# Kernel optimization log

Measured on AMD Instinct MI355X. Metric: run time of the kernel, lower is better.

The kernel has to match this reference:

```python
import jax, jax.numpy as jnp
import numpy as np

N_NODES = 100000
N_EDGES = 1600000
N_GRAPHS = 64
IN_CH = 4
HID = 64
EPS = 1e-5


def setup_inputs() -> dict:
    key = jax.random.key(0)
    ks = jax.random.split(key, 12)
    x = jax.random.normal(ks[0], (N_NODES, IN_CH), dtype=jnp.float32)
    edge_index = jax.random.randint(ks[1], (2, N_EDGES), 0, N_NODES, dtype=jnp.int32)
    batch = jnp.sort(jax.random.randint(ks[2], (N_NODES,), 0, N_GRAPHS, dtype=jnp.int32))
    s = 1.0 / np.sqrt(IN_CH)
    W_l = jax.random.uniform(ks[3], (IN_CH, HID), jnp.float32, -s, s)
    b_l = jnp.zeros((HID,), jnp.float32)
    W_r = jax.random.uniform(ks[4], (IN_CH, HID), jnp.float32, -s, s)
    b_r = jnp.zeros((HID,), jnp.float32)
    att = jax.random.normal(ks[5], (HID,), jnp.float32) / np.sqrt(HID)
    conv_bias = jnp.zeros((HID,), jnp.float32)
    ln_w = jnp.ones((HID,), jnp.float32)
    ln_b = jnp.zeros((HID,), jnp.float32)
    s2 = 1.0 / np.sqrt(HID)
    lin_w = jax.random.uniform(ks[6], (HID, 1), jnp.float32, -s2, s2)
    lin_b = jnp.zeros((1,), jnp.float32)
    return dict(x=x, edge_index=edge_index, batch=batch, W_l=W_l, b_l=b_l,
                W_r=W_r, b_r=b_r, att=att, conv_bias=conv_bias,
                ln_w=ln_w, ln_b=ln_b, lin_w=lin_w, lin_b=lin_b)


def reference(x, edge_index, batch, W_l, b_l, W_r, b_r, att, conv_bias, ln_w, ln_b, lin_w, lin_b):
    src, dst = edge_index[0], edge_index[1]  # messages flow src -> dst
    # GATv2Conv (heads=1, no self loops)
    xl = x @ W_l + b_l  # source-side transform [N, HID]
    xr = x @ W_r + b_r  # target-side transform [N, HID]
    h = xl[src] + xr[dst]                                    # [E, HID]
    e = jnp.sum(jax.nn.leaky_relu(h, 0.2) * att, axis=-1)    # [E]
    # segment softmax over incoming edges of each target node
    m = jax.ops.segment_max(e, dst, num_segments=N_NODES)
    ex = jnp.exp(e - m[dst])
    denom = jax.ops.segment_sum(ex, dst, num_segments=N_NODES)
    alpha = ex / denom[dst]                                  # [E]
    out = jax.ops.segment_sum(alpha[:, None] * xl[src], dst, num_segments=N_NODES)
    out = out + conv_bias
    out = jax.nn.relu(out)
    # PyG LayerNorm, graph mode, batch=None -> normalize over all nodes & channels
    mu = jnp.mean(out)
    var = jnp.var(out)
    out = (out - mu) / jnp.sqrt(var + EPS) * ln_w + ln_b
    # (dropout omitted: deterministic reference / eval mode)
    # global mean pool over graphs
    cnt = jax.ops.segment_sum(jnp.ones((N_NODES,), out.dtype), batch, num_segments=N_GRAPHS)
    pooled = jax.ops.segment_sum(out, batch, num_segments=N_GRAPHS) / jnp.maximum(cnt, 1.0)[:, None]
    y = pooled @ lin_w + lin_b
    return jax.nn.sigmoid(y)  # [N_GRAPHS, 1]
```

## Files before the change

### kernel.cpp

```cpp
#include <hip/hip_runtime.h>
#include <math.h>

#define N_NODES 100000
#define N_EDGES 1600000
#define N_GRAPHS 64
#define HID 64
#define LN_EPS 1e-5f
#define NB_SCAN ((N_NODES + 255) / 256)
#define KD_BLOCKS 2048
#define KD_WAVES (KD_BLOCKS * 4)
#define KD_CHUNK ((N_NODES + KD_WAVES - 1) / KD_WAVES)

__device__ __forceinline__ float waveReduceSum(float v) {
#pragma unroll
    for (int off = 32; off > 0; off >>= 1)
        v += __shfl_xor(v, off, 64);
    return v;
}

__device__ __forceinline__ float groupReduceSum16(float v) {
#pragma unroll
    for (int off = 8; off > 0; off >>= 1)
        v += __shfl_xor(v, off, 64);
    return v;
}

__device__ __forceinline__ unsigned rne_bf16(float f) {
    unsigned u = __float_as_uint(f);
    return (u + 0x7fffu + ((u >> 16) & 1u)) >> 16;
}

__global__ __launch_bounds__(256) void k0_transform(
    const float* __restrict__ x,
    const float* __restrict__ Wl, const float* __restrict__ bl,
    const float* __restrict__ Wr, const float* __restrict__ br,
    uint2* __restrict__ xlh, float4* __restrict__ xr4,
    int* __restrict__ deg,
    float* __restrict__ gsum, float* __restrict__ gcnt,
    double* __restrict__ stats) {
    if (blockIdx.x == 0) {
        for (int i = threadIdx.x; i < N_GRAPHS * HID; i += blockDim.x) gsum[i] = 0.f;
        if (threadIdx.x < N_GRAPHS) gcnt[threadIdx.x] = 0.f;
        if (threadIdx.x < 2) stats[threadIdx.x] = 0.0;
    }
    int t = blockIdx.x * blockDim.x + threadIdx.x;
    int n = t >> 4;
    int cg = t & 15;
    if (n >= N_NODES) return;
    float4 xv = ((const float4*)x)[n];
    float4 w0 = ((const float4*)Wl)[0 * 16 + cg];
    float4 w1 = ((const float4*)Wl)[1 * 16 + cg];
    float4 w2 = ((const float4*)Wl)[2 * 16 + cg];
    float4 w3 = ((const float4*)Wl)[3 * 16 + cg];
    float4 bv = ((const float4*)bl)[cg];
    float4 vl;
    vl.x = bv.x + xv.x * w0.x + xv.y * w1.x + xv.z * w2.x + xv.w * w3.x;
    vl.y = bv.y + xv.x * w0.y + xv.y * w1.y + xv.z * w2.y + xv.w * w3.y;
    vl.z = bv.z + xv.x * w0.z + xv.y * w1.z + xv.z * w2.z + xv.w * w3.z;
    vl.w = bv.w + xv.x * w0.w + xv.y * w1.w + xv.z * w2.w + xv.w * w3.w;
    w0 = ((const float4*)Wr)[0 * 16 + cg];
    w1 = ((const float4*)Wr)[1 * 16 + cg];
    w2 = ((const float4*)Wr)[2 * 16 + cg];
    w3 = ((const float4*)Wr)[3 * 16 + cg];
    bv = ((const float4*)br)[cg];
    float4 vr;
    vr.x = bv.x + xv.x * w0.x + xv.y * w1.x + xv.z * w2.x + xv.w * w3.x;
    vr.y = bv.y + xv.x * w0.y + xv.y * w1.y + xv.z * w2.y + xv.w * w3.y;
    vr.z = bv.z + xv.x * w0.z + xv.y * w1.z + xv.z * w2.z + xv.w * w3.z;
    vr.w = bv.w + xv.x * w0.w + xv.y * w1.w + xv.z * w2.w + xv.w * w3.w;
    xr4[n * 16 + cg] = vr;
    uint2 p;
    p.x = rne_bf16(vl.x) | (rne_bf16(vl.y) << 16);
    p.y = rne_bf16(vl.z) | (rne_bf16(vl.w) << 16);
    xlh[n * 16 + cg] = p;
    if (cg == 0) deg[n] = 0;
}

__global__ __launch_bounds__(256) void ka_rank(const int* __restrict__ ei,
                                               int* __restrict__ deg,
                                               int* __restrict__ erank) {
    int q = blockIdx.x * blockDim.x + threadIdx.x;
    if (q >= N_EDGES / 4) return;
    int4 d4 = ((const int4*)(ei + N_EDGES))[q];
    int4 r4;
    r4.x = atomicAdd(&deg[d4.x], 1);
    r4.y = atomicAdd(&deg[d4.y], 1);
    r4.z = atomicAdd(&deg[d4.z], 1);
    r4.w = atomicAdd(&deg[d4.w], 1);
    ((int4*)erank)[q] = r4;
}

__global__ __launch_bounds__(256) void kb1_scan(const int* __restrict__ deg,
                                                int* __restrict__ rowptr,
                                                int* __restrict__ bsum) {
    __shared__ int s[256];
    int i = blockIdx.x * 256 + threadIdx.x;
    int v = (i < N_NODES) ? deg[i] : 0;
    s[threadIdx.x] = v;
    __syncthreads();
#pragma unroll
    for (int off = 1; off < 256; off <<= 1) {
        int t = (threadIdx.x >= off) ? s[threadIdx.x - off] : 0;
        __syncthreads();
        s[threadIdx.x] += t;
        __syncthreads();
    }
    if (i < N_NODES) rowptr[i] = s[threadIdx.x] - v;
    if (threadIdx.x == 255) bsum[blockIdx.x] = s[255];
}

__global__ __launch_bounds__(512) void kb2_scan(int* __restrict__ bsum) {
    __shared__ int s[512];
    int v = (threadIdx.x < NB_SCAN) ? bsum[threadIdx.x] : 0;
    s[threadIdx.x] = v;
    __syncthreads();
#pragma unroll
    for (int off = 1; off < 512; off <<= 1) {
        int t = (threadIdx.x >= off) ? s[threadIdx.x - off] : 0;
        __syncthreads();
        s[threadIdx.x] += t;
        __syncthreads();
    }
    if (threadIdx.x < NB_SCAN) bsum[threadIdx.x] = s[threadIdx.x] - v;
}

__global__ __launch_bounds__(256) void kb3_fix(const int* __restrict__ bsum,
                                               int* __restrict__ rowptr) {
    int i = blockIdx.x * 256 + threadIdx.x;
    if (i < N_NODES) rowptr[i] = rowptr[i] + bsum[blockIdx.x];
    if (i == 0) rowptr[N_NODES] = N_EDGES;
}

__global__ __launch_bounds__(256) void kc_place(const int* __restrict__ ei,
                                                const int* __restrict__ rowptr,
                                                const int* __restrict__ erank,
                                                int* __restrict__ esrc) {
    int xcd = blockIdx.x & 7;
    int sub = blockIdx.x >> 3;
    int lo = xcd * (N_NODES / 8);
    int hi = lo + (N_NODES / 8);
    int tid = sub * 256 + (int)threadIdx.x;
    for (int q = tid; q < N_EDGES / 4; q += 64 * 256) {
        int4 d4 = ((const int4*)(ei + N_EDGES))[q];
        int4 s4 = ((const int4*)ei)[q];
        int4 r4 = ((const int4*)erank)[q];
        if (d4.x >= lo && d4.x < hi) esrc[rowptr[d4.x] + r4.x] = s4.x;
        if (d4.y >= lo && d4.y < hi) esrc[rowptr[d4.y] + r4.y] = s4.y;
        if (d4.z >= lo && d4.z < hi) esrc[rowptr[d4.z] + r4.z] = s4.z;
        if (d4.w >= lo && d4.w < hi) esrc[rowptr[d4.w] + r4.w] = s4.w;
    }
}

__global__ __launch_bounds__(256, 8) void kd_node_agg(
    const int* __restrict__ rowptr, const int* __restrict__ esrc,
    const uint2* __restrict__ xlh, const float4* __restrict__ xr4,
    const float* __restrict__ att, const float* __restrict__ cb,
    const int* __restrict__ batch,
    float* __restrict__ gsum, float* __restrict__ gcnt,
    double* __restrict__ stats) {
    __shared__ float sS[4], sQ[4];
    int w = threadIdx.x >> 6;
    int lane = threadIdx.x & 63;
    int slot = lane >> 4;
    int cg = lane & 15;
    int wid = blockIdx.x * 4 + w;
    int n0 = wid * KD_CHUNK;
    int n1 = min(n0 + KD_CHUNK, N_NODES);

    float4 av = ((const float4*)att)[cg];
    float4 cv = ((const float4*)cb)[cg];

    float lsum = 0.f, lsq = 0.f;
    float gacc0 = 0.f, gacc1 = 0.f, gacc2 = 0.f, gacc3 = 0.f;
    float runcnt = 0.f;
    int cur_g = -1;

    for (int n = n0; n < n1; ++n) {
        int beg = rowptr[n], end = rowptr[n + 1];
        float4 xr = xr4[n * 16 + cg];
        float num0 = 0.f, num1 = 0.f, num2 = 0.f, num3 = 0.f, den = 0.f;
        int j = beg + slot;
        uint2 p = make_uint2(0, 0);
        if (j < end) p = xlh[esrc[j] * 16 + cg];
        for (int j0 = beg; j0 < end; j0 += 4) {
            uint2 pc = p;
            bool vc = (j0 + slot) < end;
            int jn = j0 + 4 + slot;
            if (jn < end) p = xlh[esrc[jn] * 16 + cg];
            float f0 = __uint_as_float(pc.x << 16);
            float f1 = __uint_as_float(pc.x & 0xffff0000u);
            float f2 = __uint_as_float(pc.y << 16);
            float f3 = __uint_as_float(pc.y & 0xffff0000u);
            float h0 = f0 + xr.x, h1 = f1 + xr.y, h2 = f2 + xr.z, h3 = f3 + xr.w;
            float l0 = fmaxf(h0, 0.f) + 0.2f * fminf(h0, 0.f);
            float l1 = fmaxf(h1, 0.f) + 0.2f * fminf(h1, 0.f);
            float l2 = fmaxf(h2, 0.f) + 0.2f * fminf(h2, 0.f);
            float l3 = fmaxf(h3, 0.f) + 0.2f * fminf(h3, 0.f);
            float part = l0 * av.x + l1 * av.y + l2 * av.z + l3 * av.w;
            float e = groupReduceSum16(part);
            float ex = vc ? __expf(e) : 0.f;
            den += ex;
            num0 += ex * f0; num1 += ex * f1; num2 += ex * f2; num3 += ex * f3;
        }
#pragma unroll
        for (int off = 16; off <= 32; off <<= 1) {
            num0 += __shfl_xor(num0, off, 64);
            num1 += __shfl_xor(num1, off, 64);
            num2 += __shfl_xor(num2, off, 64);
            num3 += __shfl_xor(num3, off, 64);
            den += __shfl_xor(den, off, 64);
        }
        float inv = (den > 0.f) ? (1.f / den) : 0.f;
        float v0 = fmaxf(num0 * inv + cv.x, 0.f);
        float v1 = fmaxf(num1 * inv + cv.y, 0.f);
        float v2 = fmaxf(num2 * inv + cv.z, 0.f);
        float v3 = fmaxf(num3 * inv + cv.w, 0.f);
        if (slot == 0) {
            lsum += v0 + v1 + v2 + v3;
            lsq += v0 * v0 + v1 * v1 + v2 * v2 + v3 * v3;
            int g = batch[n];
            if (g != cur_g) {
                if (cur_g >= 0) {
                    unsafeAtomicAdd(&gsum[cur_g * HID + cg * 4 + 0], gacc0);
                    unsafeAtomicAdd(&gsum[cur_g * HID + cg * 4 + 1], gacc1);
                    unsafeAtomicAdd(&gsum[cur_g * HID + cg * 4 + 2], gacc2);
                    unsafeAtomicAdd(&gsum[cur_g * HID + cg * 4 + 3], gacc3);
                    if (cg == 0) unsafeAtomicAdd(&gcnt[cur_g], runcnt);
                }
                cur_g = g;
                gacc0 = gacc1 = gacc2 = gacc3 = 0.f;
                runcnt = 0.f;
            }
            gacc0 += v0; gacc1 += v1; gacc2 += v2; gacc3 += v3;
            runcnt += 1.f;
        }
    }
    if (cur_g >= 0) {
        unsafeAtomicAdd(&gsum[cur_g * HID + cg * 4 + 0], gacc0);
        unsafeAtomicAdd(&gsum[cur_g * HID + cg * 4 + 1], gacc1);
        unsafeAtomicAdd(&gsum[cur_g * HID + cg * 4 + 2], gacc2);
        unsafeAtomicAdd(&gsum[cur_g * HID + cg * 4 + 3], gacc3);
        if (cg == 0) unsafeAtomicAdd(&gcnt[cur_g], runcnt);
    }
    lsum = groupReduceSum16(lsum);
    lsq = groupReduceSum16(lsq);
    if (lane == 0) { sS[w] = lsum; sQ[w] = lsq; }
    __syncthreads();
    if (threadIdx.x == 0) {
        double ds = 0.0, dq = 0.0;
#pragma unroll
        for (int i = 0; i < 4; ++i) { ds += (double)sS[i]; dq += (double)sQ[i]; }
        unsafeAtomicAdd(&stats[0], ds);
        unsafeAtomicAdd(&stats[1], dq);
    }
}

__global__ __launch_bounds__(64) void k4_head(
    const float* __restrict__ gsum, const float* __restrict__ gcnt,
    const double* __restrict__ stats,
    const float* __restrict__ lnw, const float* __restrict__ lnb,
    const float* __restrict__ linw, const float* __restrict__ linb,
    float* __restrict__ y) {
    int g = blockIdx.x;
    int lane = threadIdx.x;
    double tot = (double)N_NODES * (double)HID;
    double mu = stats[0] / tot;
    double var = stats[1] / tot - mu * mu;
    float rs = rsqrtf((float)var + LN_EPS);
    float cnt = fmaxf(gcnt[g], 1.f);
    float pooled = (gsum[g * HID + lane] / cnt - (float)mu) * rs * lnw[lane] + lnb[lane];
    float t = waveReduceSum(pooled * linw[lane]);
    if (lane == 0) {
        float z = t + linb[0];
        y[g] = 1.f / (1.f + __expf(-z));
    }
}

extern "C" void kernel_launch(void* const* d_in, const int* in_sizes, int n_in,
                              void* d_out, int out_size, void* d_ws, size_t ws_size,
                              hipStream_t stream) {
    const float* x = (const float*)d_in[0];
    const int* ei = (const int*)d_in[1];
    const int* batch = (const int*)d_in[2];
    const float* Wl = (const float*)d_in[3];
    const float* bl = (const float*)d_in[4];
    const float* Wr = (const float*)d_in[5];
    const float* br = (const float*)d_in[6];
    const float* att = (const float*)d_in[7];
    const float* cb = (const float*)d_in[8];
    const float* lnw = (const float*)d_in[9];
    const float* lnb = (const float*)d_in[10];
    const float* linw = (const float*)d_in[11];
    const float* linb = (const float*)d_in[12];
    float* y = (float*)d_out;

    char* ws = (char*)d_ws;
    float4* xr4 = (float4*)ws;
    uint2* xlh = (uint2*)(ws + (size_t)N_NODES * 16 * 16);
    float* gsum = (float*)((char*)xlh + (size_t)N_NODES * 16 * 8);
    float* gcnt = gsum + N_GRAPHS * HID;
    double* stats = (double*)(gcnt + N_GRAPHS);
    int* rowptr = (int*)(stats + 2);
    int* deg = rowptr + (N_NODES + 1);
    int* bsum = deg + N_NODES;
    int* erank = bsum + 512;
    int* esrc = erank + N_EDGES;

    k0_transform<<<(N_NODES * 16 + 255) / 256, 256, 0, stream>>>(
        x, Wl, bl, Wr, br, xlh, xr4, deg, gsum, gcnt, stats);
    ka_rank<<<(N_EDGES / 4 + 255) / 256, 256, 0, stream>>>(ei, deg, erank);
    kb1_scan<<<NB_SCAN, 256, 0, stream>>>(deg, rowptr, bsum);
    kb2_scan<<<1, 512, 0, stream>>>(bsum);
    kb3_fix<<<NB_SCAN, 256, 0, stream>>>(bsum, rowptr);
    kc_place<<<512, 256, 0, stream>>>(ei, rowptr, erank, esrc);
    kd_node_agg<<<KD_BLOCKS, 256, 0, stream>>>(
        rowptr, esrc, xlh, xr4, att, cb, batch, gsum, gcnt, stats);
    k4_head<<<N_GRAPHS, 64, 0, stream>>>(gsum, gcnt, stats, lnw, lnb, linw, linb, y);
}
```

Before: 325.0 us.

## Fuse scan fixup and head into consumers, widen aggregation to 8 channels per lane

Drops the kb3_fix kernel by adding the block offset bsum when rowptr is read in kc_place and kd_node_agg. Merges the head kernel into the aggregation kernel through a last-block atomic counter with threadfences. Each lane now handles 8 bf16 channels with uint4 loads, so 8 edges run in parallel per wave. The 16-lane reduction becomes an 8-lane one, and launch bounds occupancy drops from 8 to 6. kc_place now reads src and rank as scalars instead of int4, and the head runs serially in a single block.

```diff
diff --git a/kernel.cpp b/kernel.cpp
--- a/kernel.cpp
+++ b/kernel.cpp
@@ -18,13 +18,6 @@
     return v;
 }
 
-__device__ __forceinline__ float groupReduceSum16(float v) {
-#pragma unroll
-    for (int off = 8; off > 0; off >>= 1)
-        v += __shfl_xor(v, off, 64);
-    return v;
-}
-
 __device__ __forceinline__ unsigned rne_bf16(float f) {
     unsigned u = __float_as_uint(f);
     return (u + 0x7fffu + ((u >> 16) & 1u)) >> 16;
@@ -37,11 +30,12 @@
     uint2* __restrict__ xlh, float4* __restrict__ xr4,
     int* __restrict__ deg,
     float* __restrict__ gsum, float* __restrict__ gcnt,
-    double* __restrict__ stats) {
+    double* __restrict__ stats, int* __restrict__ ctr) {
     if (blockIdx.x == 0) {
         for (int i = threadIdx.x; i < N_GRAPHS * HID; i += blockDim.x) gsum[i] = 0.f;
         if (threadIdx.x < N_GRAPHS) gcnt[threadIdx.x] = 0.f;
         if (threadIdx.x < 2) stats[threadIdx.x] = 0.0;
+        if (threadIdx.x == 0) *ctr = 0;
     }
     int t = blockIdx.x * blockDim.x + threadIdx.x;
     int n = t >> 4;
@@ -124,15 +118,9 @@
     if (threadIdx.x < NB_SCAN) bsum[threadIdx.x] = s[threadIdx.x] - v;
 }
 
-__global__ __launch_bounds__(256) void kb3_fix(const int* __restrict__ bsum,
-                                               int* __restrict__ rowptr) {
-    int i = blockIdx.x * 256 + threadIdx.x;
-    if (i < N_NODES) rowptr[i] = rowptr[i] + bsum[blockIdx.x];
-    if (i == 0) rowptr[N_NODES] = N_EDGES;
-}
-
 __global__ __launch_bounds__(256) void kc_place(const int* __restrict__ ei,
                                                 const int* __restrict__ rowptr,
+                                                const int* __restrict__ bsum,
                                                 const int* __restrict__ erank,
                                                 int* __restrict__ esrc) {
     int xcd = blockIdx.x & 7;
@@ -142,108 +130,140 @@
     int tid = sub * 256 + (int)threadIdx.x;
     for (int q = tid; q < N_EDGES / 4; q += 64 * 256) {
         int4 d4 = ((const int4*)(ei + N_EDGES))[q];
-        int4 s4 = ((const int4*)ei)[q];
-        int4 r4 = ((const int4*)erank)[q];
-        if (d4.x >= lo && d4.x < hi) esrc[rowptr[d4.x] + r4.x] = s4.x;
-        if (d4.y >= lo && d4.y < hi) esrc[rowptr[d4.y] + r4.y] = s4.y;
-        if (d4.z >= lo && d4.z < hi) esrc[rowptr[d4.z] + r4.z] = s4.z;
-        if (d4.w >= lo && d4.w < hi) esrc[rowptr[d4.w] + r4.w] = s4.w;
-    }
-}
-
-__global__ __launch_bounds__(256, 8) void kd_node_agg(
-    const int* __restrict__ rowptr, const int* __restrict__ esrc,
-    const uint2* __restrict__ xlh, const float4* __restrict__ xr4,
+        int i0 = q * 4;
+        if (d4.x >= lo && d4.x < hi)
+            esrc[rowptr[d4.x] + bsum[d4.x >> 8] + erank[i0 + 0]] = ei[i0 + 0];
+        if (d4.y >= lo && d4.y < hi)
+            esrc[rowptr[d4.y] + bsum[d4.y >> 8] + erank[i0 + 1]] = ei[i0 + 1];
+        if (d4.z >= lo && d4.z < hi)
+            esrc[rowptr[d4.z] + bsum[d4.z >> 8] + erank[i0 + 2]] = ei[i0 + 2];
+        if (d4.w >= lo && d4.w < hi)
+            esrc[rowptr[d4.w] + bsum[d4.w >> 8] + erank[i0 + 3]] = ei[i0 + 3];
+    }
+}
+
+__global__ __launch_bounds__(256, 6) void kd_node_agg(
+    const int* __restrict__ rowptr, const int* __restrict__ bsum,
+    const int* __restrict__ esrc,
+    const uint4* __restrict__ xlh4, const float4* __restrict__ xr4,
     const float* __restrict__ att, const float* __restrict__ cb,
     const int* __restrict__ batch,
     float* __restrict__ gsum, float* __restrict__ gcnt,
-    double* __restrict__ stats) {
+    double* __restrict__ stats, int* __restrict__ ctr,
+    const float* __restrict__ lnw, const float* __restrict__ lnb,
+    const float* __restrict__ linw, const float* __restrict__ linb,
+    float* __restrict__ y) {
     __shared__ float sS[4], sQ[4];
+    __shared__ int sLast;
     int w = threadIdx.x >> 6;
     int lane = threadIdx.x & 63;
-    int slot = lane >> 4;
-    int cg = lane & 15;
+    int slot = lane >> 3;
+    int cg = lane & 7;
     int wid = blockIdx.x * 4 + w;
     int n0 = wid * KD_CHUNK;
     int n1 = min(n0 + KD_CHUNK, N_NODES);
 
-    float4 av = ((const float4*)att)[cg];
-    float4 cv = ((const float4*)cb)[cg];
+    float av[8], cv[8];
+    {
+        float4 a0 = ((const float4*)att)[cg * 2], a1 = ((const float4*)att)[cg * 2 + 1];
+        av[0] = a0.x; av[1] = a0.y; av[2] = a0.z; av[3] = a0.w;
+        av[4] = a1.x; av[5] = a1.y; av[6] = a1.z; av[7] = a1.w;
+        float4 c0 = ((const float4*)cb)[cg * 2], c1 = ((const float4*)cb)[cg * 2 + 1];
+        cv[0] = c0.x; cv[1] = c0.y; cv[2] = c0.z; cv[3] = c0.w;
+        cv[4] = c1.x; cv[5] = c1.y; cv[6] = c1.z; cv[7] = c1.w;
+    }
 
     float lsum = 0.f, lsq = 0.f;
-    float gacc0 = 0.f, gacc1 = 0.f, gacc2 = 0.f, gacc3 = 0.f;
+    float gacc[8] = {0.f, 0.f, 0.f, 0.f, 0.f, 0.f, 0.f, 0.f};
     float runcnt = 0.f;
     int cur_g = -1;
 
     for (int n = n0; n < n1; ++n) {
-        int beg = rowptr[n], end = rowptr[n + 1];
-        float4 xr = xr4[n * 16 + cg];
-        float num0 = 0.f, num1 = 0.f, num2 = 0.f, num3 = 0.f, den = 0.f;
+        int beg = rowptr[n] + bsum[n >> 8];
+        int end = (n + 1 < N_NODES) ? (rowptr[n + 1] + bsum[(n + 1) >> 8]) : N_EDGES;
+        float xr[8];
+        {
+            float4 r0 = xr4[n * 16 + cg * 2], r1 = xr4[n * 16 + cg * 2 + 1];
+            xr[0] = r0.x; xr[1] = r0.y; xr[2] = r0.z; xr[3] = r0.w;
+            xr[4] = r1.x; xr[5] = r1.y; xr[6] = r1.z; xr[7] = r1.w;
+        }
+        float num[8] = {0.f, 0.f, 0.f, 0.f, 0.f, 0.f, 0.f, 0.f};
+        float den = 0.f;
         int j = beg + slot;
-        uint2 p = make_uint2(0, 0);
-        if (j < end) p = xlh[esrc[j] * 16 + cg];
-        for (int j0 = beg; j0 < end; j0 += 4) {
-            uint2 pc = p;
+        uint4 p = make_uint4(0, 0, 0, 0);
+        if (j < end) p = xlh4[esrc[j] * 8 + cg];
+        for (int j0 = beg; j0 < end; j0 += 8) {
+            uint4 pc = p;
             bool vc = (j0 + slot) < end;
-            int jn = j0 + 4 + slot;
-            if (jn < end) p = xlh[esrc[jn] * 16 + cg];
-            float f0 = __uint_as_float(pc.x << 16);
-            float f1 = __uint_as_float(pc.x & 0xffff0000u);
-            float f2 = __uint_as_float(pc.y << 16);
-            float f3 = __uint_as_float(pc.y & 0xffff0000u);
-            float h0 = f0 + xr.x, h1 = f1 + xr.y, h2 = f2 + xr.z, h3 = f3 + xr.w;
-            float l0 = fmaxf(h0, 0.f) + 0.2f * fminf(h0, 0.f);
-            float l1 = fmaxf(h1, 0.f) + 0.2f * fminf(h1, 0.f);
-            float l2 = fmaxf(h2, 0.f) + 0.2f * fminf(h2, 0.f);
-            float l3 = fmaxf(h3, 0.f) + 0.2f * fminf(h3, 0.f);
-            float part = l0 * av.x + l1 * av.y + l2 * av.z + l3 * av.w;
-            float e = groupReduceSum16(part);
-            float ex = vc ? __expf(e) : 0.f;
+            int jn = j0 + 8 + slot;
+            if (jn < end) p = xlh4[esrc[jn] * 8 + cg];
+            float f[8];
+            f[0] = __uint_as_float(pc.x << 16);
+            f[1] = __uint_as_float(pc.x & 0xffff0000u);
+            f[2] = __uint_as_float(pc.y << 16);
+            f[3] = __uint_as_float(pc.y & 0xffff0000u);
+            f[4] = __uint_as_float(pc.z << 16);
+            f[5] = __uint_as_float(pc.z & 0xffff0000u);
+            f[6] = __uint_as_float(pc.w << 16);
+            f[7] = __uint_as_float(pc.w & 0xffff0000u);
+            float part = 0.f;
+#pragma unroll
+            for (int k = 0; k < 8; ++k) {
+                float h = f[k] + xr[k];
+                float l = fmaxf(h, 0.f) + 0.2f * fminf(h, 0.f);
+                part += l * av[k];
+            }
+            part += __shfl_xor(part, 1, 64);
+            part += __shfl_xor(part, 2, 64);
+            part += __shfl_xor(part, 4, 64);
+            float ex = vc ? __expf(part) : 0.f;
             den += ex;
-            num0 += ex * f0; num1 += ex * f1; num2 += ex * f2; num3 += ex * f3;
-        }
-#pragma unroll
-        for (int off = 16; off <= 32; off <<= 1) {
-            num0 += __shfl_xor(num0, off, 64);
-            num1 += __shfl_xor(num1, off, 64);
-            num2 += __shfl_xor(num2, off, 64);
-            num3 += __shfl_xor(num3, off, 64);
+#pragma unroll
+            for (int k = 0; k < 8; ++k) num[k] += ex * f[k];
+        }
+#pragma unroll
+        for (int off = 8; off <= 32; off <<= 1) {
+#pragma unroll
+            for (int k = 0; k < 8; ++k) num[k] += __shfl_xor(num[k], off, 64);
             den += __shfl_xor(den, off, 64);
         }
         float inv = (den > 0.f) ? (1.f / den) : 0.f;
-        float v0 = fmaxf(num0 * inv + cv.x, 0.f);
-        float v1 = fmaxf(num1 * inv + cv.y, 0.f);
-        float v2 = fmaxf(num2 * inv + cv.z, 0.f);
-        float v3 = fmaxf(num3 * inv + cv.w, 0.f);
         if (slot == 0) {
-            lsum += v0 + v1 + v2 + v3;
-            lsq += v0 * v0 + v1 * v1 + v2 * v2 + v3 * v3;
             int g = batch[n];
             if (g != cur_g) {
                 if (cur_g >= 0) {
-                    unsafeAtomicAdd(&gsum[cur_g * HID + cg * 4 + 0], gacc0);
-                    unsafeAtomicAdd(&gsum[cur_g * HID + cg * 4 + 1], gacc1);
-                    unsafeAtomicAdd(&gsum[cur_g * HID + cg * 4 + 2], gacc2);
-                    unsafeAtomicAdd(&gsum[cur_g * HID + cg * 4 + 3], gacc3);
+#pragma unroll
+                    for (int k = 0; k < 8; ++k)
+                        unsafeAtomicAdd(&gsum[cur_g * HID + cg * 8 + k], gacc[k]);
                     if (cg == 0) unsafeAtomicAdd(&gcnt[cur_g], runcnt);
                 }
                 cur_g = g;
-                gacc0 = gacc1 = gacc2 = gacc3 = 0.f;
+#pragma unroll
+                for (int k = 0; k < 8; ++k) gacc[k] = 0.f;
                 runcnt = 0.f;
             }
-            gacc0 += v0; gacc1 += v1; gacc2 += v2; gacc3 += v3;
+#pragma unroll
+            for (int k = 0; k < 8; ++k) {
+                float v = fmaxf(num[k] * inv + cv[k], 0.f);
+                lsum += v;
+                lsq += v * v;
+                gacc[k] += v;
+            }
             runcnt += 1.f;
         }
     }
     if (cur_g >= 0) {
-        unsafeAtomicAdd(&gsum[cur_g * HID + cg * 4 + 0], gacc0);
-        unsafeAtomicAdd(&gsum[cur_g * HID + cg * 4 + 1], gacc1);
-        unsafeAtomicAdd(&gsum[cur_g * HID + cg * 4 + 2], gacc2);
-        unsafeAtomicAdd(&gsum[cur_g * HID + cg * 4 + 3], gacc3);
+#pragma unroll
+        for (int k = 0; k < 8; ++k)
+            unsafeAtomicAdd(&gsum[cur_g * HID + cg * 8 + k], gacc[k]);
         if (cg == 0) unsafeAtomicAdd(&gcnt[cur_g], runcnt);
     }
-    lsum = groupReduceSum16(lsum);
-    lsq = groupReduceSum16(lsq);
+    lsum += __shfl_xor(lsum, 1, 64);
+    lsum += __shfl_xor(lsum, 2, 64);
+    lsum += __shfl_xor(lsum, 4, 64);
+    lsq += __shfl_xor(lsq, 1, 64);
+    lsq += __shfl_xor(lsq, 2, 64);
+    lsq += __shfl_xor(lsq, 4, 64);
     if (lane == 0) { sS[w] = lsum; sQ[w] = lsq; }
     __syncthreads();
     if (threadIdx.x == 0) {
@@ -253,26 +273,27 @@
         unsafeAtomicAdd(&stats[0], ds);
         unsafeAtomicAdd(&stats[1], dq);
     }
-}
-
-__global__ __launch_bounds__(64) void k4_head(
-    const float* __restrict__ gsum, const float* __restrict__ gcnt,
-    const double* __restrict__ stats,
-    const float* __restrict__ lnw, const float* __restrict__ lnb,
-    const float* __restrict__ linw, const float* __restrict__ linb,
-    float* __restrict__ y) {
-    int g = blockIdx.x;
-    int lane = threadIdx.x;
-    double tot = (double)N_NODES * (double)HID;
-    double mu = stats[0] / tot;
-    double var = stats[1] / tot - mu * mu;
-    float rs = rsqrtf((float)var + LN_EPS);
-    float cnt = fmaxf(gcnt[g], 1.f);
-    float pooled = (gsum[g * HID + lane] / cnt - (float)mu) * rs * lnw[lane] + lnb[lane];
-    float t = waveReduceSum(pooled * linw[lane]);
-    if (lane == 0) {
-        float z = t + linb[0];
-        y[g] = 1.f / (1.f + __expf(-z));
+    __threadfence();
+    if (threadIdx.x == 0) {
+        int t = atomicAdd(ctr, 1);
+        sLast = (t == KD_BLOCKS - 1) ? 1 : 0;
+    }
+    __syncthreads();
+    if (sLast) {
+        __threadfence();
+        double tot = (double)N_NODES * (double)HID;
+        double mu = stats[0] / tot;
+        double var = stats[1] / tot - mu * mu;
+        float rs = rsqrtf((float)var + LN_EPS);
+        int l64 = threadIdx.x & 63;
+        int wv = threadIdx.x >> 6;
+        for (int g = wv * 16; g < wv * 16 + 16; ++g) {
+            float cnt = fmaxf(gcnt[g], 1.f);
+            float pooled =
+                (gsum[g * HID + l64] / cnt - (float)mu) * rs * lnw[l64] + lnb[l64];
+            float t = waveReduceSum(pooled * linw[l64]);
+            if (l64 == 0) y[g] = 1.f / (1.f + __expf(-(t + linb[0])));
+        }
     }
 }
 
@@ -296,24 +317,24 @@
 
     char* ws = (char*)d_ws;
     float4* xr4 = (float4*)ws;
-    uint2* xlh = (uint2*)(ws + (size_t)N_NODES * 16 * 16);
-    float* gsum = (float*)((char*)xlh + (size_t)N_NODES * 16 * 8);
+    uint2* xlh = (uint2*)(ws + (size_t)N_NODES * 256);
+    float* gsum = (float*)((char*)xlh + (size_t)N_NODES * 128);
     float* gcnt = gsum + N_GRAPHS * HID;
     double* stats = (double*)(gcnt + N_GRAPHS);
-    int* rowptr = (int*)(stats + 2);
+    int* ctr = (int*)(stats + 2);
+    int* rowptr = ctr + 2;
     int* deg = rowptr + (N_NODES + 1);
     int* bsum = deg + N_NODES;
     int* erank = bsum + 512;
     int* esrc = erank + N_EDGES;
 
     k0_transform<<<(N_NODES * 16 + 255) / 256, 256, 0, stream>>>(
-        x, Wl, bl, Wr, br, xlh, xr4, deg, gsum, gcnt, stats);
+        x, Wl, bl, Wr, br, xlh, xr4, deg, gsum, gcnt, stats, ctr);
     ka_rank<<<(N_EDGES / 4 + 255) / 256, 256, 0, stream>>>(ei, deg, erank);
     kb1_scan<<<NB_SCAN, 256, 0, stream>>>(deg, rowptr, bsum);
     kb2_scan<<<1, 512, 0, stream>>>(bsum);
-    kb3_fix<<<NB_SCAN, 256, 0, stream>>>(bsum, rowptr);
-    kc_place<<<512, 256, 0, stream>>>(ei, rowptr, erank, esrc);
+    kc_place<<<512, 256, 0, stream>>>(ei, rowptr, bsum, erank, esrc);
     kd_node_agg<<<KD_BLOCKS, 256, 0, stream>>>(
-        rowptr, esrc, xlh, xr4, att, cb, batch, gsum, gcnt, stats);
-    k4_head<<<N_GRAPHS, 64, 0, stream>>>(gsum, gcnt, stats, lnw, lnb, linw, linb, y);
-}
+        rowptr, bsum, esrc, (const uint4*)xlh, xr4, att, cb, batch,
+        gsum, gcnt, stats, ctr, lnw, lnb, linw, linb, y);
+}
```

After: 540.5 us. 1.66x slower.
